# Kernel optimization log

Hardware: AMD Instinct MI355X
Metric: run time of the kernel (lower is better)

## Reference

```python
import jax, jax.numpy as jnp
import numpy as np

N_HEADS = 12
B, S, D = 2, 2048, 768
NEG = -1e9


def setup_inputs() -> dict:
    key = jax.random.key(0)
    ks = jax.random.split(key, 7)
    scale = 1.0 / np.sqrt(D)
    Q = jax.random.normal(ks[0], (B, S, D), jnp.float32)
    K = jax.random.normal(ks[1], (B, S, D), jnp.float32)
    V = jax.random.normal(ks[2], (B, S, D), jnp.float32)
    # causal mask, broadcastable over batch and heads; 0 entries are masked out
    mask = jnp.tril(jnp.ones((S, S), jnp.int32))[None, None, :, :]
    Wq = jax.random.normal(ks[3], (D, D), jnp.float32) * scale
    Wk = jax.random.normal(ks[4], (D, D), jnp.float32) * scale
    Wv = jax.random.normal(ks[5], (D, D), jnp.float32) * scale
    Wo = jax.random.normal(ks[6], (D, D), jnp.float32) * scale
    return {"Q": Q, "K": K, "V": V, "mask": mask,
            "Wq": Wq, "Wk": Wk, "Wv": Wv, "Wo": Wo}


def reference(Q, K, V, mask, Wq, Wk, Wv, Wo):
    b, s, d = Q.shape
    h = N_HEADS
    dk = d // h
    # projections (torch nn.Linear: x @ W.T), split heads -> (b, h, s, dk)
    q = (Q @ Wq.T).reshape(b, s, h, dk).transpose(0, 2, 1, 3)
    k = (K @ Wk.T).reshape(b, s, h, dk).transpose(0, 2, 1, 3)
    v = (V @ Wv.T).reshape(b, s, h, dk).transpose(0, 2, 1, 3)
    scores = jnp.einsum('bhqd,bhkd->bhqk', q, k) / jnp.sqrt(jnp.asarray(dk, q.dtype))
    scores = jnp.where(mask == 0, jnp.asarray(NEG, scores.dtype), scores)
    attn = jax.nn.softmax(scores, axis=-1)  # dropout p=0.0 -> identity
    ctx = jnp.einsum('bhqk,bhkd->bhqd', attn, v)
    ctx = ctx.transpose(0, 2, 1, 3).reshape(b, s, d)
    return ctx @ Wo.T
```

## Files before the change

### kernel.cpp

```cpp
#include <hip/hip_runtime.h>
#include <math.h>

#define NH     12
#define BB     2
#define SEQ    2048
#define DMODEL 768
#define DK     64

typedef __attribute__((ext_vector_type(8))) short short8;
typedef __attribute__((ext_vector_type(4))) short short4v;
typedef __attribute__((ext_vector_type(4))) float floatx4;

__device__ __forceinline__ unsigned short f2bf(float x) {
    unsigned u = __builtin_bit_cast(unsigned, x);
    u = (u + 0x7fffu + ((u >> 16) & 1u)) >> 16;
    return (unsigned short)u;
}
__device__ __forceinline__ unsigned short f2bf_fast(float x) {
    unsigned u = __builtin_bit_cast(unsigned, x);
    return (unsigned short)((u + 0x8000u) >> 16);
}
__device__ __forceinline__ float bf2f(unsigned short h) {
    unsigned u = ((unsigned)h) << 16;
    return __builtin_bit_cast(float, u);
}

__device__ __forceinline__ void gld_lds16(const ushort* gptr, ushort* lptr) {
    __builtin_amdgcn_global_load_lds(
        (const __attribute__((address_space(1))) unsigned int*)(const void*)gptr,
        (__attribute__((address_space(3))) unsigned int*)(void*)lptr,
        16, 0, 0);
}

__device__ __forceinline__ short4v shfl8(short4v v, int src) {
    int2 t = __builtin_bit_cast(int2, v);
    t.x = __shfl(t.x, src);
    t.y = __shfl(t.y, src);
    return __builtin_bit_cast(short4v, t);
}

#define SI (BB * SEQ * DMODEL)
#define SW (DMODEL * DMODEL)

#define P1_BLOCKS 1024

__global__ __launch_bounds__(256) void cast_w(
    const float* __restrict__ Wq, const float* __restrict__ Wk,
    const float* __restrict__ Wv, const float* __restrict__ Wo,
    ushort* oWq, ushort* oWk, ushort* oWv, ushort* oWo, int* counter) {
    if (blockIdx.x == 0 && threadIdx.x == 0) *counter = P1_BLOCKS;
    long i = (long)(blockIdx.x * 256 + threadIdx.x) * 4;
    const float* src; ushort* dst; long off;
    if      (i < 1L * SW) { src = Wq; dst = oWq; off = i; }
    else if (i < 2L * SW) { src = Wk; dst = oWk; off = i - 1L * SW; }
    else if (i < 3L * SW) { src = Wv; dst = oWv; off = i - 2L * SW; }
    else                  { src = Wo; dst = oWo; off = i - 3L * SW; }
    float4 v = *(const float4*)(src + off);
    ushort4 o;
    o.x = f2bf(v.x); o.y = f2bf(v.y); o.z = f2bf(v.z); o.w = f2bf(v.w);
    *(ushort4*)(dst + off) = o;
}

template<int MODE, bool AF32, int TM>
__device__ __forceinline__ void gemm_body(ushort* __restrict__ Sbase,
                                          const void* __restrict__ Av,
                                          const ushort* __restrict__ W,
                                          float* __restrict__ outF,
                                          ushort* __restrict__ outH,
                                          float scale) {
    constexpr int ATS = TM * 32;
    constexpr int BST = ATS + 128 * 32;
    constexpr int MI  = TM / 32;
    constexpr int AIT = TM / 64;
    constexpr int NWG = (TM == 128) ? 192 : 384;

    const int lin = blockIdx.y * 6 + blockIdx.x;
    const int swz = (lin & 7) * (NWG / 8) + (lin >> 3);
    const int n0 = (swz % 6) * 128;
    const int m0 = (swz / 6) * TM;

    const int tid  = threadIdx.x;
    const int lane = tid & 63;
    const int wv   = tid >> 6;
    const int l15  = lane & 15;
    const int quad = lane >> 4;
    const int wm = (wv >> 1) * (TM / 2);
    const int wn = (wv & 1) * 64;

    const int srow = tid >> 2;
    const int sch  = tid & 3;
    const int schx = sch ^ ((srow >> 1) & 3);
    const int sw2  = (l15 >> 1) & 3;

    const ushort* Ab = (const ushort*)Av;
    const float*  Af = (const float*)Av;

    floatx4 acc[MI][4];
    #pragma unroll
    for (int i = 0; i < MI; ++i)
        #pragma unroll
        for (int j = 0; j < 4; ++j) acc[i][j] = (floatx4)0.f;

    float4 ar0[2], ar1[2];
    #pragma unroll
    for (int it = 0; it < AIT; ++it) {
        const int r = srow + it * 64;
        if (AF32) {
            const float* p = Af + (size_t)(m0 + r) * DMODEL + schx * 8;
            ar0[it] = *(const float4*)p;
            ar1[it] = *(const float4*)(p + 4);
        } else {
            gld_lds16(Ab + (size_t)(m0 + r) * DMODEL + schx * 8, Sbase + r * 32 + sch * 8);
        }
    }
    #pragma unroll
    for (int it = 0; it < 2; ++it) {
        const int r = srow + it * 64;
        gld_lds16(W + (size_t)(n0 + r) * DMODEL + schx * 8, Sbase + ATS + r * 32 + sch * 8);
    }
    if (AF32) {
        #pragma unroll
        for (int it = 0; it < AIT; ++it) {
            const int r = srow + it * 64;
            short8 s8;
            s8[0] = (short)f2bf_fast(ar0[it].x); s8[1] = (short)f2bf_fast(ar0[it].y);
            s8[2] = (short)f2bf_fast(ar0[it].z); s8[3] = (short)f2bf_fast(ar0[it].w);
            s8[4] = (short)f2bf_fast(ar1[it].x); s8[5] = (short)f2bf_fast(ar1[it].y);
            s8[6] = (short)f2bf_fast(ar1[it].z); s8[7] = (short)f2bf_fast(ar1[it].w);
            *(short8*)(Sbase + r * 32 + sch * 8) = s8;
        }
    }

    const int NS = DMODEL / 32;
    for (int t = 0; t < NS; ++t) {
        __syncthreads();
        const int bi = (t + 1) & 1;
        ushort* SbufN = Sbase + bi * BST;
        if (t + 1 < NS) {
            const int k0 = (t + 1) * 32;
            #pragma unroll
            for (int it = 0; it < AIT; ++it) {
                const int r = srow + it * 64;
                if (AF32) {
                    const float* p = Af + (size_t)(m0 + r) * DMODEL + k0 + schx * 8;
                    ar0[it] = *(const float4*)p;
                    ar1[it] = *(const float4*)(p + 4);
                } else {
                    gld_lds16(Ab + (size_t)(m0 + r) * DMODEL + k0 + schx * 8, SbufN + r * 32 + sch * 8);
                }
            }
            #pragma unroll
            for (int it = 0; it < 2; ++it) {
                const int r = srow + it * 64;
                gld_lds16(W + (size_t)(n0 + r) * DMODEL + k0 + schx * 8, SbufN + ATS + r * 32 + sch * 8);
            }
        }
        const ushort* As  = Sbase + (t & 1) * BST;
        const ushort* Ws2 = As + ATS;
        short8 af[MI], bf[4];
        #pragma unroll
        for (int mi = 0; mi < MI; ++mi)
            af[mi] = *(const short8*)&As[(wm + mi * 16 + l15) * 32 + ((quad ^ sw2) * 8)];
        #pragma unroll
        for (int ni = 0; ni < 4; ++ni)
            bf[ni] = *(const short8*)&Ws2[(wn + ni * 16 + l15) * 32 + ((quad ^ sw2) * 8)];
        #pragma unroll
        for (int mi = 0; mi < MI; ++mi)
            #pragma unroll
            for (int ni = 0; ni < 4; ++ni) {
                if (MODE == 2)
                    acc[mi][ni] = __builtin_amdgcn_mfma_f32_16x16x32_bf16(bf[ni], af[mi], acc[mi][ni], 0, 0, 0);
                else
                    acc[mi][ni] = __builtin_amdgcn_mfma_f32_16x16x32_bf16(af[mi], bf[ni], acc[mi][ni], 0, 0, 0);
            }
        if (AF32 && t + 1 < NS) {
            #pragma unroll
            for (int it = 0; it < AIT; ++it) {
                const int r = srow + it * 64;
                short8 s8;
                s8[0] = (short)f2bf_fast(ar0[it].x); s8[1] = (short)f2bf_fast(ar0[it].y);
                s8[2] = (short)f2bf_fast(ar0[it].z); s8[3] = (short)f2bf_fast(ar0[it].w);
                s8[4] = (short)f2bf_fast(ar1[it].x); s8[5] = (short)f2bf_fast(ar1[it].y);
                s8[6] = (short)f2bf_fast(ar1[it].z); s8[7] = (short)f2bf_fast(ar1[it].w);
                *(short8*)(SbufN + r * 32 + sch * 8) = s8;
            }
        }
    }

    #pragma unroll
    for (int mi = 0; mi < MI; ++mi)
        #pragma unroll
        for (int ni = 0; ni < 4; ++ni)
            #pragma unroll
            for (int r = 0; r < 4; ++r) {
                const float v = acc[mi][ni][r] * scale;
                if (MODE == 2) {
                    const int m = m0 + wm + mi * 16 + l15;
                    const int n = n0 + wn + ni * 16 + quad * 4 + r;
                    const int b = m >> 11, s = m & (SEQ - 1);
                    const int h = n >> 6,  dk = n & 63;
                    outH[(((size_t)b * NH + h) * DK + dk) * SEQ + s] = f2bf(v);
                } else {
                    const int m = m0 + wm + mi * 16 + quad * 4 + r;
                    const int n = n0 + wn + ni * 16 + l15;
                    if (MODE == 0) {
                        outF[(size_t)m * DMODEL + n] = v;
                    } else {
                        const int b = m >> 11, s = m & (SEQ - 1);
                        const int h = n >> 6,  dk = n & 63;
                        outH[(((size_t)b * NH + h) * SEQ + s) * DK + dk] = f2bf(v);
                    }
                }
            }
}

#define QSCALE (0.125f * 1.44269504088896f)

__global__ __launch_bounds__(256) void gemm_qkv(
    const float* Q, const float* K, const float* V,
    const ushort* Wqb, const ushort* Wkb, const ushort* Wvb,
    ushort* qh, ushort* kh, ushort* vhT) {
    __shared__ __align__(16) ushort S[2 * (128 * 32 + 128 * 32)];
    const int z = blockIdx.z;
    if (z == 0)      gemm_body<1, true, 128>(S, Q, Wqb, nullptr, qh,  QSCALE);
    else if (z == 1) gemm_body<1, true, 128>(S, K, Wkb, nullptr, kh,  1.0f);
    else             gemm_body<2, true, 128>(S, V, Wvb, nullptr, vhT, 1.0f);
}

__global__ __launch_bounds__(256) void gemm_out(const ushort* A, const ushort* W, float* out) {
    __shared__ __align__(16) ushort S[2 * (64 * 32 + 128 * 32)];
    gemm_body<0, false, 64>(S, A, W, out, nullptr, 1.0f);
}

#define NIT   (24 * 72)
#define MBIAS -20.0f
__device__ const int d_offs[17] = {0,1,2,4,6,9,12,16,20,25,30,36,42,49,56,64,72};

__global__ __launch_bounds__(256, 4) void flash_p1(const ushort* __restrict__ qh,
                                                   const ushort* __restrict__ kh,
                                                   const ushort* __restrict__ vhT,
                                                   ushort* __restrict__ ctx,
                                                   ushort* __restrict__ Opart,
                                                   float* __restrict__ lpart,
                                                   int* __restrict__ counter) {
    const int tid  = threadIdx.x;
    const int lane = tid & 63;
    const int wv   = tid >> 6;
    const int l15  = lane & 15;
    const int quad = lane >> 4;

    __shared__ __align__(16) ushort KV[2][2][64 * 64];
    __shared__ int wshare;

    const int srow = tid >> 3;
    const int sch  = tid & 7;
    const int schx = sch ^ (srow & 7);
    const int swq  = l15 & 7;

    const int srcA = l15 + 32 * (quad & 1);
    const int srcB = srcA + 16;
    const bool hiq = (quad >> 1) != 0;

    int w = blockIdx.x;
    for (;;) {
        if (w >= NIT) break;
        if (tid == 0) wshare = atomicAdd(counter, 1);
        const int bh = w / 72;
        const int r72 = w - bh * 72;
        int Q = 0;
        #pragma unroll
        for (int q = 0; q < 16; ++q) if (r72 >= d_offs[q + 1]) Q = q + 1;
        const int s  = r72 - d_offs[Q];
        const int ns = (Q >> 1) + 1;
        const int b  = bh / NH, h = bh % NH;
        const int qbase = Q * 128;
        const int k_lo = 4 * s;
        const int k_hi = min(4 * s + 3, 2 * Q + 1);

        const ushort* kbase = kh  + (size_t)bh * SEQ * DK;
        const ushort* vbase = vhT + (size_t)bh * DK * SEQ;

        short8 qf[2][2];
        #pragma unroll
        for (int qs = 0; qs < 2; ++qs) {
            const ushort* qp = qh + ((size_t)bh * SEQ + qbase + wv * 32 + qs * 16 + l15) * DK;
            qf[qs][0] = *(const short8*)(qp + quad * 8);
            qf[qs][1] = *(const short8*)(qp + 32 + quad * 8);
        }

        {
            const int k0 = k_lo * 64;
            gld_lds16(kbase + (size_t)(k0 + srow) * DK + schx * 8,        &KV[0][0][srow * 64 + sch * 8]);
            gld_lds16(kbase + (size_t)(k0 + srow + 32) * DK + schx * 8,   &KV[0][0][(srow + 32) * 64 + sch * 8]);
            gld_lds16(vbase + (size_t)srow * SEQ + k0 + schx * 8,         &KV[0][1][srow * 64 + sch * 8]);
            gld_lds16(vbase + (size_t)(srow + 32) * SEQ + k0 + schx * 8,  &KV[0][1][(srow + 32) * 64 + sch * 8]);
        }

        float l_s[2] = {0.f, 0.f};
        floatx4 o_acc[2][4];
        #pragma unroll
        for (int qs = 0; qs < 2; ++qs)
            #pragma unroll
            for (int d = 0; d < 4; ++d) o_acc[qs][d] = (floatx4)0.f;

        for (int kt = k_lo; kt <= k_hi; ++kt) {
            __syncthreads();
            if (kt < k_hi) {
                const int k0 = (kt + 1) * 64;
                const int bi = (kt + 1 - k_lo) & 1;
                gld_lds16(kbase + (size_t)(k0 + srow) * DK + schx * 8,        &KV[bi][0][srow * 64 + sch * 8]);
                gld_lds16(kbase + (size_t)(k0 + srow + 32) * DK + schx * 8,   &KV[bi][0][(srow + 32) * 64 + sch * 8]);
                gld_lds16(vbase + (size_t)srow * SEQ + k0 + schx * 8,         &KV[bi][1][srow * 64 + sch * 8]);
                gld_lds16(vbase + (size_t)(srow + 32) * SEQ + k0 + schx * 8,  &KV[bi][1][(srow + 32) * 64 + sch * 8]);
            }
            const int cb = (kt - k_lo) & 1;
            const ushort* Ks  = KV[cb][0];
            const ushort* Vts = KV[cb][1];
            const bool diag = (kt >= 2 * Q);

            #pragma unroll
            for (int qs = 0; qs < 2; ++qs) {
                floatx4 s_acc[4];
                #pragma unroll
                for (int nt = 0; nt < 4; ++nt) s_acc[nt] = (floatx4)(MBIAS);
                #pragma unroll
                for (int kc = 0; kc < 2; ++kc)
                    #pragma unroll
                    for (int nt = 0; nt < 4; ++nt) {
                        short8 kf = *(const short8*)&Ks[(nt * 16 + l15) * 64 + (((kc * 4 + quad) ^ swq) * 8)];
                        s_acc[nt] = __builtin_amdgcn_mfma_f32_16x16x32_bf16(kf, qf[qs][kc], s_acc[nt], 0, 0, 0);
                    }

                if (diag) {
                    const int qg = qbase + wv * 32 + qs * 16 + l15;
                    #pragma unroll
                    for (int nt = 0; nt < 4; ++nt)
                        #pragma unroll
                        for (int rr = 0; rr < 4; ++rr)
                            if (kt * 64 + nt * 16 + quad * 4 + rr > qg) s_acc[nt][rr] = -1.0e30f;
                }

                float lp0 = 0.f, lp1 = 0.f, lp2 = 0.f, lp3 = 0.f;
                short4v packed[4];
                #pragma unroll
                for (int nt = 0; nt < 4; ++nt)
                    #pragma unroll
                    for (int rr = 0; rr < 4; ++rr) {
                        const float p = exp2f(s_acc[nt][rr]);
                        if      (rr == 0) lp0 += p;
                        else if (rr == 1) lp1 += p;
                        else if (rr == 2) lp2 += p;
                        else              lp3 += p;
                        packed[nt][rr] = (short)f2bf_fast(p);
                    }
                l_s[qs] += (lp0 + lp1) + (lp2 + lp3);

                #pragma unroll
                for (int kc = 0; kc < 2; ++kc) {
                    short4v a0 = shfl8(packed[2 * kc],     srcA);
                    short4v a1 = shfl8(packed[2 * kc + 1], srcA);
                    short4v b0 = shfl8(packed[2 * kc],     srcB);
                    short4v b1 = shfl8(packed[2 * kc + 1], srcB);
                    short4v lo = hiq ? a1 : a0;
                    short4v hi = hiq ? b1 : b0;
                    short8 pf;
                    pf[0] = lo[0]; pf[1] = lo[1]; pf[2] = lo[2]; pf[3] = lo[3];
                    pf[4] = hi[0]; pf[5] = hi[1]; pf[6] = hi[2]; pf[7] = hi[3];
                    #pragma unroll
                    for (int dkt = 0; dkt < 4; ++dkt) {
                        short8 vf = *(const short8*)&Vts[(dkt * 16 + l15) * 64 + (((kc * 4 + quad) ^ swq) * 8)];
                        o_acc[qs][dkt] = __builtin_amdgcn_mfma_f32_16x16x32_bf16(pf, vf, o_acc[qs][dkt], 0, 0, 0);
                    }
                }
            }
        }

        #pragma unroll
        for (int qs = 0; qs < 2; ++qs) {
            l_s[qs] += __shfl_xor(l_s[qs], 16);
            l_s[qs] += __shfl_xor(l_s[qs], 32);
        }

        if (ns == 1) {
            #pragma unroll
            for (int qs = 0; qs < 2; ++qs)
                #pragma unroll
                for (int rr = 0; rr < 4; ++rr) {
                    const float lr = __shfl(l_s[qs], quad * 20 + rr);
                    const float inv = 1.f / lr;
                    const int sg = qbase + wv * 32 + qs * 16 + quad * 4 + rr;
                    #pragma unroll
                    for (int dkt = 0; dkt < 4; ++dkt) {
                        const int d = h * DK + dkt * 16 + l15;
                        ctx[((size_t)b * SEQ + sg) * DMODEL + d] = f2bf(o_acc[qs][dkt][rr] * inv);
                    }
                }
        } else {
            const int pid = bh * 70 + (d_offs[Q] - 2) + s;
            ushort* op = Opart + (size_t)pid * (128 * 64);
            #pragma unroll
            for (int qs = 0; qs < 2; ++qs) {
                #pragma unroll
                for (int rr = 0; rr < 4; ++rr) {
                    const int row = wv * 32 + qs * 16 + quad * 4 + rr;
                    #pragma unroll
                    for (int dkt = 0; dkt < 4; ++dkt)
                        op[row * 64 + dkt * 16 + l15] = f2bf(o_acc[qs][dkt][rr]);
                }
                if (quad == 0)
                    lpart[(size_t)pid * 128 + wv * 32 + qs * 16 + l15] = l_s[qs];
            }
        }

        w = wshare;
        __syncthreads();
    }
}

__global__ __launch_bounds__(256) void flash_combine(const ushort* __restrict__ Opart,
                                                     const float* __restrict__ lpart,
                                                     ushort* __restrict__ ctx) {
    const int bh = blockIdx.x / 14;
    const int Q  = 2 + blockIdx.x % 14;
    const int ns = (Q >> 1) + 1;
    const int pbase = bh * 70 + (d_offs[Q] - 2);
    const int b = bh / NH, h = bh % NH;
    const int t = threadIdx.x;
    const int row = t >> 1;
    const int c0  = (t & 1) * 32;

    float lt = 0.f;
    for (int s2 = 0; s2 < ns; ++s2) lt += lpart[(size_t)(pbase + s2) * 128 + row];
    const float inv = 1.f / lt;

    float acc[32];
    #pragma unroll
    for (int j = 0; j < 32; ++j) acc[j] = 0.f;
    for (int s2 = 0; s2 < ns; ++s2) {
        const ushort* op = Opart + (size_t)(pbase + s2) * (128 * 64) + row * 64 + c0;
        #pragma unroll
        for (int j = 0; j < 32; j += 8) {
            short8 v = *(const short8*)(op + j);
            #pragma unroll
            for (int e = 0; e < 8; ++e) acc[j + e] += bf2f((unsigned short)v[e]);
        }
    }
    ushort* dst = ctx + ((size_t)b * SEQ + Q * 128 + row) * DMODEL + h * DK + c0;
    #pragma unroll
    for (int j = 0; j < 32; j += 8) {
        short8 o;
        #pragma unroll
        for (int e = 0; e < 8; ++e) o[e] = (short)f2bf(acc[j + e] * inv);
        *(short8*)(dst + j) = o;
    }
}

extern "C" void kernel_launch(void* const* d_in, const int* in_sizes, int n_in,
                              void* d_out, int out_size, void* d_ws, size_t ws_size,
                              hipStream_t stream) {
    const float* Q  = (const float*)d_in[0];
    const float* K  = (const float*)d_in[1];
    const float* V  = (const float*)d_in[2];
    const float* Wq = (const float*)d_in[4];
    const float* Wk = (const float*)d_in[5];
    const float* Wv = (const float*)d_in[6];
    const float* Wo = (const float*)d_in[7];

    char* ws = (char*)d_ws;
    const size_t SZ_IN = (size_t)SI * 2;
    const size_t SZ_W  = (size_t)SW * 2;
    ushort* Wqb   = (ushort*)(ws);
    ushort* Wkb   = (ushort*)(ws + SZ_W);
    ushort* Wvb   = (ushort*)(ws + 2 * SZ_W);
    ushort* Wob   = (ushort*)(ws + 3 * SZ_W);
    ushort* qh    = (ushort*)(ws + 4 * SZ_W);
    ushort* kh    = (ushort*)(ws + 4 * SZ_W + SZ_IN);
    ushort* vhT   = (ushort*)(ws + 4 * SZ_W + 2 * SZ_IN);
    ushort* ctx   = (ushort*)(ws + 4 * SZ_W + 3 * SZ_IN);
    ushort* Opart = (ushort*)(ws + 4 * SZ_W + 4 * SZ_IN);
    float*  lpart = (float*) (ws + 4 * SZ_W + 4 * SZ_IN + (size_t)1680 * 8192 * 2);
    int*    ctr   = (int*)   (ws + 4 * SZ_W + 4 * SZ_IN + (size_t)1680 * 8192 * 2
                                 + (size_t)1680 * 128 * 4);

    dim3 blk(256);
    cast_w<<<dim3(4 * SW / 1024), blk, 0, stream>>>(Wq, Wk, Wv, Wo,
                                                    Wqb, Wkb, Wvb, Wob, ctr);
    gemm_qkv<<<dim3(6, 32, 3), blk, 0, stream>>>(Q, K, V, Wqb, Wkb, Wvb, qh, kh, vhT);
    flash_p1<<<dim3(P1_BLOCKS), blk, 0, stream>>>(qh, kh, vhT, ctx, Opart, lpart, ctr);
    flash_combine<<<dim3(24 * 14), blk, 0, stream>>>(Opart, lpart, ctx);
    gemm_out<<<dim3(6, 64), blk, 0, stream>>>(ctx, Wob, (float*)d_out);
}
```

Baseline: 211.2 us.

## Share K/V LDS fragments across both query subtiles and reverse work order

Interleaves the two query subtiles inside the attention inner loop so each K and V fragment read from shared memory feeds two MFMAs instead of one, halving LDS reads. Swizzled column offsets are precomputed once per thread. The persistent work queue is walked in reverse so the longest (diagonal-heavy) items are scheduled first for better load balance. The work index is made wave-uniform with readfirstlane. Register pressure rises because both subtiles' score accumulators are live at once.

```diff
diff --git a/kernel.cpp b/kernel.cpp
--- a/kernel.cpp
+++ b/kernel.cpp
@@ -261,12 +261,15 @@
     const int srcB = srcA + 16;
     const bool hiq = (quad >> 1) != 0;
 
+    const int colc[2] = { ((quad ^ swq) * 8), (((4 + quad) ^ swq) * 8) };
+
     int w = blockIdx.x;
     for (;;) {
         if (w >= NIT) break;
         if (tid == 0) wshare = atomicAdd(counter, 1);
-        const int bh = w / 72;
-        const int r72 = w - bh * 72;
+        const int item = NIT - 1 - w;
+        const int bh = item / 72;
+        const int r72 = item - bh * 72;
         int Q = 0;
         #pragma unroll
         for (int q = 0; q < 16; ++q) if (r72 >= d_offs[q + 1]) Q = q + 1;
@@ -318,59 +321,69 @@
             const ushort* Vts = KV[cb][1];
             const bool diag = (kt >= 2 * Q);
 
-            #pragma unroll
-            for (int qs = 0; qs < 2; ++qs) {
-                floatx4 s_acc[4];
-                #pragma unroll
-                for (int nt = 0; nt < 4; ++nt) s_acc[nt] = (floatx4)(MBIAS);
-                #pragma unroll
-                for (int kc = 0; kc < 2; ++kc)
-                    #pragma unroll
-                    for (int nt = 0; nt < 4; ++nt) {
-                        short8 kf = *(const short8*)&Ks[(nt * 16 + l15) * 64 + (((kc * 4 + quad) ^ swq) * 8)];
-                        s_acc[nt] = __builtin_amdgcn_mfma_f32_16x16x32_bf16(kf, qf[qs][kc], s_acc[nt], 0, 0, 0);
-                    }
-
-                if (diag) {
+            floatx4 s_acc[2][4];
+            #pragma unroll
+            for (int qs = 0; qs < 2; ++qs)
+                #pragma unroll
+                for (int nt = 0; nt < 4; ++nt) s_acc[qs][nt] = (floatx4)(MBIAS);
+            #pragma unroll
+            for (int kc = 0; kc < 2; ++kc)
+                #pragma unroll
+                for (int nt = 0; nt < 4; ++nt) {
+                    short8 kf = *(const short8*)&Ks[(nt * 16 + l15) * 64 + colc[kc]];
+                    s_acc[0][nt] = __builtin_amdgcn_mfma_f32_16x16x32_bf16(kf, qf[0][kc], s_acc[0][nt], 0, 0, 0);
+                    s_acc[1][nt] = __builtin_amdgcn_mfma_f32_16x16x32_bf16(kf, qf[1][kc], s_acc[1][nt], 0, 0, 0);
+                }
+
+            if (diag) {
+                #pragma unroll
+                for (int qs = 0; qs < 2; ++qs) {
                     const int qg = qbase + wv * 32 + qs * 16 + l15;
                     #pragma unroll
                     for (int nt = 0; nt < 4; ++nt)
                         #pragma unroll
                         for (int rr = 0; rr < 4; ++rr)
-                            if (kt * 64 + nt * 16 + quad * 4 + rr > qg) s_acc[nt][rr] = -1.0e30f;
-                }
-
+                            if (kt * 64 + nt * 16 + quad * 4 + rr > qg) s_acc[qs][nt][rr] = -1.0e30f;
+                }
+            }
+
+            short4v packed[2][4];
+            #pragma unroll
+            for (int qs = 0; qs < 2; ++qs) {
                 float lp0 = 0.f, lp1 = 0.f, lp2 = 0.f, lp3 = 0.f;
-                short4v packed[4];
                 #pragma unroll
                 for (int nt = 0; nt < 4; ++nt)
                     #pragma unroll
                     for (int rr = 0; rr < 4; ++rr) {
-                        const float p = exp2f(s_acc[nt][rr]);
+                        const float p = exp2f(s_acc[qs][nt][rr]);
                         if      (rr == 0) lp0 += p;
                         else if (rr == 1) lp1 += p;
                         else if (rr == 2) lp2 += p;
                         else              lp3 += p;
-                        packed[nt][rr] = (short)f2bf_fast(p);
+                        packed[qs][nt][rr] = (short)f2bf_fast(p);
                     }
                 l_s[qs] += (lp0 + lp1) + (lp2 + lp3);
-
-                #pragma unroll
-                for (int kc = 0; kc < 2; ++kc) {
-                    short4v a0 = shfl8(packed[2 * kc],     srcA);
-                    short4v a1 = shfl8(packed[2 * kc + 1], srcA);
-                    short4v b0 = shfl8(packed[2 * kc],     srcB);
-                    short4v b1 = shfl8(packed[2 * kc + 1], srcB);
+            }
+
+            #pragma unroll
+            for (int kc = 0; kc < 2; ++kc) {
+                short8 pf[2];
+                #pragma unroll
+                for (int qs = 0; qs < 2; ++qs) {
+                    short4v a0 = shfl8(packed[qs][2 * kc],     srcA);
+                    short4v a1 = shfl8(packed[qs][2 * kc + 1], srcA);
+                    short4v b0 = shfl8(packed[qs][2 * kc],     srcB);
+                    short4v b1 = shfl8(packed[qs][2 * kc + 1], srcB);
                     short4v lo = hiq ? a1 : a0;
                     short4v hi = hiq ? b1 : b0;
-                    short8 pf;
-                    pf[0] = lo[0]; pf[1] = lo[1]; pf[2] = lo[2]; pf[3] = lo[3];
-                    pf[4] = hi[0]; pf[5] = hi[1]; pf[6] = hi[2]; pf[7] = hi[3];
-                    #pragma unroll
-                    for (int dkt = 0; dkt < 4; ++dkt) {
-                        short8 vf = *(const short8*)&Vts[(dkt * 16 + l15) * 64 + (((kc * 4 + quad) ^ swq) * 8)];
-                        o_acc[qs][dkt] = __builtin_amdgcn_mfma_f32_16x16x32_bf16(pf, vf, o_acc[qs][dkt], 0, 0, 0);
-                    }
+                    pf[qs][0] = lo[0]; pf[qs][1] = lo[1]; pf[qs][2] = lo[2]; pf[qs][3] = lo[3];
+                    pf[qs][4] = hi[0]; pf[qs][5] = hi[1]; pf[qs][6] = hi[2]; pf[qs][7] = hi[3];
+                }
+                #pragma unroll
+                for (int dkt = 0; dkt < 4; ++dkt) {
+                    short8 vf = *(const short8*)&Vts[(dkt * 16 + l15) * 64 + colc[kc]];
+                    o_acc[0][dkt] = __builtin_amdgcn_mfma_f32_16x16x32_bf16(pf[0], vf, o_acc[0][dkt], 0, 0, 0);
+                    o_acc[1][dkt] = __builtin_amdgcn_mfma_f32_16x16x32_bf16(pf[1], vf, o_acc[1][dkt], 0, 0, 0);
                 }
             }
         }
@@ -412,7 +425,7 @@
             }
         }
 
-        w = wshare;
+        w = __builtin_amdgcn_readfirstlane(wshare);
         __syncthreads();
     }
 }
```

Measured after the change: 208.5 us. No clear change (-1.3%).
